# Optimization experiments

Measured on AMD Instinct MI355X. Metric: run time of the kernel, lower is better.

Reference implementation:

```python
import jax, jax.numpy as jnp
import numpy as np

B, S, HID = 1, 2048, 1024
H, HKV, D = 16, 4, 64
THETA = 10000.0


def _rope_tables(seq_len, head_dim):
    # Matches RotaryEmbedding: emb = cat(freqs, freqs); kernel reads cos/sin at even
    # positions d for each rotated pair (d, d+1), i.e. columns 0::2 of the table.
    inv_freq = 1.0 / (THETA ** (jnp.arange(0, head_dim, 2, dtype=jnp.float32) / head_dim))
    freqs = jnp.arange(seq_len, dtype=jnp.float32)[:, None] * inv_freq[None, :]  # [S, D/2]
    emb = jnp.concatenate([freqs, freqs], axis=-1)  # [S, D]
    return jnp.cos(emb)[:, 0::2], jnp.sin(emb)[:, 0::2]  # each [S, D/2]


def _apply_rope(x, cos, sin):
    # x: [B, H, S, D]; rotate interleaved pairs (2i, 2i+1) as in the kernel.
    xe, xo = x[..., 0::2], x[..., 1::2]
    re = xe * cos - xo * sin
    ro = xe * sin + xo * cos
    return jnp.stack([re, ro], axis=-1).reshape(x.shape)


def setup_inputs() -> dict:
    key = jax.random.key(0)
    k0, k1, k2, k3, k4 = jax.random.split(key, 5)
    return {
        "hidden_states": jax.random.normal(k0, (B, S, HID), dtype=jnp.float32),
        "Wq": jax.random.normal(k1, (HID, H * D), dtype=jnp.float32) * 0.02,
        "Wk": jax.random.normal(k2, (HID, HKV * D), dtype=jnp.float32) * 0.02,
        "Wv": jax.random.normal(k3, (HID, HKV * D), dtype=jnp.float32) * 0.02,
        "Wo": jax.random.normal(k4, (H * D, HID), dtype=jnp.float32) * 0.02,
    }


def reference(hidden_states, Wq, Wk, Wv, Wo):
    b, s, _ = hidden_states.shape
    q = (hidden_states @ Wq).reshape(b, s, H, D).transpose(0, 2, 1, 3)    # [B,H,S,D]
    k = (hidden_states @ Wk).reshape(b, s, HKV, D).transpose(0, 2, 1, 3)  # [B,Hkv,S,D]
    v = (hidden_states @ Wv).reshape(b, s, HKV, D).transpose(0, 2, 1, 3)

    cos, sin = _rope_tables(s, D)
    q = _apply_rope(q, cos, sin)
    k = _apply_rope(k, cos, sin)

    G = H // HKV  # GQA group size: query head h -> kv head h // G
    qg = q.reshape(b, HKV, G, s, D)
    scale = jnp.float32(D) ** -0.5
    scores = jnp.einsum("bkgqd,bkpd->bkgqp", qg, k) * scale  # [B,Hkv,G,S,S]
    causal = jnp.tril(jnp.ones((s, s), dtype=bool))
    scores = jnp.where(causal, scores, jnp.float32(-1e30))
    probs = jax.nn.softmax(scores, axis=-1)
    out = jnp.einsum("bkgqp,bkpd->bkgqd", probs, v).reshape(b, H, s, D)
    out = out.transpose(0, 2, 1, 3).reshape(b, s, H * D)
    return out @ Wo
```

## Files before the change

### kernel.cpp

```cpp
#include <hip/hip_runtime.h>
#include <hip/hip_bf16.h>
#include <math.h>

#define SEQ   2048
#define HID   1024
#define NH    16
#define NKV   4
#define DH    64
#define GQ    (NH / NKV)
#define NQKV  1536
#define KT    64
#define QB    32
#define CH    512
#define NCH   (SEQ / CH)
#define PSTR  72
#define LNSC  0.2878231366f

typedef __attribute__((ext_vector_type(8))) short bf16x8;
typedef __attribute__((ext_vector_type(4))) float f32x4;
typedef unsigned short u16;
typedef unsigned int u32;

__device__ __forceinline__ u16 f2bf(float f) {
    union { float f; unsigned u; } x; x.f = f;
    unsigned r = x.u + 0x7fffu + ((x.u >> 16) & 1u);
    return (u16)(r >> 16);
}
__device__ __forceinline__ u32 pk2bf(float lo, float hi) {
    return (u32)f2bf(lo) | ((u32)f2bf(hi) << 16);
}
__device__ __forceinline__ void load_lds16(const u16* g, u16* l) {
    __builtin_amdgcn_global_load_lds(
        (const __attribute__((address_space(1))) unsigned int*)g,
        (__attribute__((address_space(3))) unsigned int*)l, 16, 0, 0);
}

__global__ __launch_bounds__(256) void setup(const float* __restrict__ X,
                                             const float* __restrict__ Wq,
                                             const float* __restrict__ Wk,
                                             const float* __restrict__ Wv,
                                             const float* __restrict__ Wo,
                                             u16* __restrict__ Xb,
                                             u16* __restrict__ Wt,
                                             u16* __restrict__ WoT) {
    const int z = blockIdx.z;
    if (z == 4) {
        const int idx = ((int)blockIdx.y * 64 + (int)blockIdx.x) * 256 + threadIdx.x;
        const float4 v = ((const float4*)X)[idx];
        ushort4 o;
        o.x = f2bf(v.x); o.y = f2bf(v.y); o.z = f2bf(v.z); o.w = f2bf(v.w);
        ((ushort4*)Xb)[idx] = o;
        return;
    }
    const float* in; u16* out; int N;
    if (z == 0)      { in = Wq; out = Wt;                             N = HID; }
    else if (z == 1) { in = Wk; out = Wt + (size_t)HID * HID;         N = 256; }
    else if (z == 2) { in = Wv; out = Wt + (size_t)(HID + 256) * HID; N = 256; }
    else             { in = Wo; out = WoT;                            N = HID; }

    const int n0 = blockIdx.x * 32;
    if (n0 >= N) return;
    const int k0 = blockIdx.y * 32;

    __shared__ float t[32][33];
    const int tx = threadIdx.x & 31;
    const int ty = threadIdx.x >> 5;
    #pragma unroll
    for (int i = 0; i < 4; ++i)
        t[ty + i * 8][tx] = in[(size_t)(k0 + ty + i * 8) * N + n0 + tx];
    __syncthreads();
    #pragma unroll
    for (int i = 0; i < 4; ++i)
        out[(size_t)(n0 + ty + i * 8) * HID + k0 + tx] = f2bf(t[tx][ty + i * 8]);
}

__global__ __launch_bounds__(256) void gemm_qkv(const u16* __restrict__ A,
                                                const u16* __restrict__ Bt,
                                                u16* __restrict__ Qb,
                                                u16* __restrict__ Kb,
                                                u16* __restrict__ VTg) {
    __shared__ u16 Bs[2][64 * 32];

    const int tid  = threadIdx.x;
    const int lane = tid & 63;
    const int w    = tid >> 6;
    const int c    = lane & 15;
    const int quad = lane >> 4;
    const int m0   = blockIdx.y * 64;
    const int n0   = blockIdx.x * 64;

    const u16* gB  = Bt + (size_t)(n0 + w * 16 + (lane >> 2)) * HID + (lane & 3) * 8;
    u16* const bdst = (u16*)&Bs[0][0] + (w * 16) * 32;
    const u16* gA = A + (size_t)(m0 + w * 16 + c) * HID + quad * 8;

    f32x4 acc[4];
    #pragma unroll
    for (int nt = 0; nt < 4; ++nt) acc[nt] = (f32x4){0.f, 0.f, 0.f, 0.f};

    bf16x8 afc, afn;
    afc = *(const bf16x8*)gA;
    load_lds16(gB, bdst);

    for (int t = 0; t < HID / 32; ++t) {
        __syncthreads();
        if (t + 1 < HID / 32) {
            load_lds16(gB + (t + 1) * 32, bdst + ((t + 1) & 1) * (64 * 32));
            afn = *(const bf16x8*)(gA + (t + 1) * 32);
        }
        bf16x8 bfr[4];
        #pragma unroll
        for (int nt = 0; nt < 4; ++nt)
            bfr[nt] = *(const bf16x8*)&Bs[t & 1][(nt * 16 + c) * 32 + quad * 8];
        #pragma unroll
        for (int nt = 0; nt < 4; ++nt)
            acc[nt] = __builtin_amdgcn_mfma_f32_16x16x32_bf16(afc, bfr[nt], acc[nt], 0, 0, 0);
        afc = afn;
    }

    const int s0 = m0 + w * 16 + quad * 4;
    if (n0 < 1280) {
        const bool isQ = (n0 < 1024);
        #pragma unroll
        for (int nt = 0; nt < 4; ++nt) {
            const int d = nt * 16 + c;
            const float inv_freq = __expf(-(float)(d & 30) * LNSC);
            const float sgn = (d & 1) ? 1.f : -1.f;
            #pragma unroll
            for (int rg = 0; rg < 4; ++rg) {
                const float self = acc[nt][rg];
                const float partner = __shfl_xor(self, 1);
                float sn, cs;
                __sincosf((float)(s0 + rg) * inv_freq, &sn, &cs);
                float o = fmaf(partner, sgn * sn, self * cs);
                if (isQ) {
                    Qb[(size_t)(s0 + rg) * HID + n0 + d] = f2bf(o * 0.125f);
                } else {
                    const int kh = (n0 - 1024) >> 6;
                    Kb[((size_t)kh * SEQ + s0 + rg) * DH + d] = f2bf(o);
                }
            }
        }
    } else {
        const int kh = (n0 - 1280) >> 6;
        #pragma unroll
        for (int nt = 0; nt < 4; ++nt) {
            const int d = nt * 16 + c;
            ushort4 o;
            o.x = f2bf(acc[nt][0]); o.y = f2bf(acc[nt][1]);
            o.z = f2bf(acc[nt][2]); o.w = f2bf(acc[nt][3]);
            *(ushort4*)&VTg[((size_t)kh * DH + d) * SEQ + s0] = o;
        }
    }
}

__global__ __launch_bounds__(256) void gemm64(const u16* __restrict__ A,
                                              const u16* __restrict__ Bt,
                                              float* __restrict__ C,
                                              int K, int ldc) {
    __shared__ u16 Bs[2][64 * 32];

    const int tid  = threadIdx.x;
    const int lane = tid & 63;
    const int w    = tid >> 6;
    const int c    = lane & 15;
    const int quad = lane >> 4;
    const int m0   = blockIdx.y * 64;
    const int n0   = blockIdx.x * 64;

    const u16* gB  = Bt + (size_t)(n0 + w * 16 + (lane >> 2)) * K + (lane & 3) * 8;
    u16* const bdst = (u16*)&Bs[0][0] + (w * 16) * 32;
    const u16* gA = A + (size_t)(m0 + w * 16 + c) * K + quad * 8;

    const int T = K / 32;

    f32x4 acc[4];
    #pragma unroll
    for (int nt = 0; nt < 4; ++nt) acc[nt] = (f32x4){0.f, 0.f, 0.f, 0.f};

    bf16x8 afc, afn;
    afc = *(const bf16x8*)gA;
    load_lds16(gB, bdst);

    for (int t = 0; t < T; ++t) {
        __syncthreads();
        if (t + 1 < T) {
            load_lds16(gB + (t + 1) * 32, bdst + ((t + 1) & 1) * (64 * 32));
            afn = *(const bf16x8*)(gA + (t + 1) * 32);
        }
        bf16x8 bfr[4];
        #pragma unroll
        for (int nt = 0; nt < 4; ++nt)
            bfr[nt] = *(const bf16x8*)&Bs[t & 1][(nt * 16 + c) * 32 + quad * 8];
        #pragma unroll
        for (int nt = 0; nt < 4; ++nt)
            acc[nt] = __builtin_amdgcn_mfma_f32_16x16x32_bf16(afc, bfr[nt], acc[nt], 0, 0, 0);
        afc = afn;
    }

    #pragma unroll
    for (int nt = 0; nt < 4; ++nt)
        #pragma unroll
        for (int rg = 0; rg < 4; ++rg)
            C[(size_t)(m0 + w * 16 + quad * 4 + rg) * ldc + n0 + nt * 16 + c] = acc[nt][rg];
}

__global__ __launch_bounds__(256) void attn_kernel(const u16* __restrict__ Qb,
                                                   const u16* __restrict__ Kb,
                                                   const u16* __restrict__ VTg,
                                                   float* __restrict__ Opart,
                                                   float* __restrict__ lpart) {
    __shared__ u16 Ks[2][2][64 * 32];
    __shared__ u16 Vs[2][2][64 * 32];
    __shared__ u16 Pst[4][QB * PSTR];

    const int tid  = threadIdx.x;
    const int lane = tid & 63;
    const int w    = tid >> 6;
    const int c    = lane & 15;
    const int quad = lane >> 4;
    const int kh   = blockIdx.y;
    const int z    = blockIdx.z;
    const int qt   = (SEQ / QB - 1) - (int)blockIdx.x;
    const int q0   = qt * QB;
    const int h    = kh * GQ + w;

    const int kstart = z * CH;
    const int klim   = q0 + QB;
    if (kstart >= klim) return;
    const int kend   = (klim < kstart + CH) ? klim : (kstart + CH);
    const int ntiles = (kend - kstart + KT - 1) / KT;

    bf16x8 qf[2][2];
    #pragma unroll
    for (int g = 0; g < 2; ++g)
        #pragma unroll
        for (int ks = 0; ks < 2; ++ks)
            qf[g][ks] = *(const bf16x8*)&Qb[(size_t)(q0 + g * 16 + c) * HID + h * DH + ks * 32 + quad * 8];

    f32x4 accO[4][2];
    #pragma unroll
    for (int nt = 0; nt < 4; ++nt)
        #pragma unroll
        for (int g = 0; g < 2; ++g)
            accO[nt][g] = (f32x4){0.f, 0.f, 0.f, 0.f};
    float l[2] = {0.f, 0.f};

    const int hf = w >> 1;
    const int g0 = (w & 1) * 2;
    const int srow = (lane >> 2);
    const int scol = (lane & 3) * 8;

    {
        #pragma unroll
        for (int gi = 0; gi < 2; ++gi) {
            const int g = g0 + gi;
            load_lds16(Kb + ((size_t)kh * SEQ + kstart + g * 16 + srow) * DH + hf * 32 + scol,
                       &Ks[0][hf][(g * 16) * 32]);
            load_lds16(VTg + ((size_t)kh * DH + g * 16 + srow) * SEQ + kstart + hf * 32 + scol,
                       &Vs[0][hf][(g * 16) * 32]);
        }
    }

    for (int t = 0; t < ntiles; ++t) {
        const int kt0 = kstart + t * KT;
        __syncthreads();
        if (t + 1 < ntiles) {
            const int nk = kt0 + KT;
            const int nb = (t + 1) & 1;
            #pragma unroll
            for (int gi = 0; gi < 2; ++gi) {
                const int g = g0 + gi;
                load_lds16(Kb + ((size_t)kh * SEQ + nk + g * 16 + srow) * DH + hf * 32 + scol,
                           &Ks[nb][hf][(g * 16) * 32]);
                load_lds16(VTg + ((size_t)kh * DH + g * 16 + srow) * SEQ + nk + hf * 32 + scol,
                           &Vs[nb][hf][(g * 16) * 32]);
            }
        }
        const int b = t & 1;

        f32x4 accS[4][2];
        #pragma unroll
        for (int nS = 0; nS < 4; ++nS)
            #pragma unroll
            for (int g = 0; g < 2; ++g)
                accS[nS][g] = (f32x4){0.f, 0.f, 0.f, 0.f};
        #pragma unroll
        for (int nS = 0; nS < 4; ++nS)
            #pragma unroll
            for (int ks = 0; ks < 2; ++ks) {
                const bf16x8 kf = *(const bf16x8*)&Ks[b][ks][(nS * 16 + c) * 32 + quad * 8];
                #pragma unroll
                for (int g = 0; g < 2; ++g)
                    accS[nS][g] = __builtin_amdgcn_mfma_f32_16x16x32_bf16(kf, qf[g][ks], accS[nS][g], 0, 0, 0);
            }

        #pragma unroll
        for (int g = 0; g < 2; ++g) {
            const int q = q0 + g * 16 + c;
            #pragma unroll
            for (int nS = 0; nS < 4; ++nS) {
                const int key = kt0 + nS * 16 + quad * 4;
                const float p0 = (key + 0 <= q) ? __expf(accS[nS][g][0]) : 0.f;
                const float p1 = (key + 1 <= q) ? __expf(accS[nS][g][1]) : 0.f;
                const float p2 = (key + 2 <= q) ? __expf(accS[nS][g][2]) : 0.f;
                const float p3 = (key + 3 <= q) ? __expf(accS[nS][g][3]) : 0.f;
                l[g] += (p0 + p1) + (p2 + p3);
                u32* dst = (u32*)&Pst[w][(g * 16 + c) * PSTR + nS * 16 + quad * 4];
                dst[0] = pk2bf(p0, p1);
                dst[1] = pk2bf(p2, p3);
            }
        }
        __threadfence_block();

        #pragma unroll
        for (int ks2 = 0; ks2 < 2; ++ks2) {
            bf16x8 pf[2];
            #pragma unroll
            for (int g = 0; g < 2; ++g)
                pf[g] = *(const bf16x8*)&Pst[w][(g * 16 + c) * PSTR + ks2 * 32 + quad * 8];
            #pragma unroll
            for (int nt = 0; nt < 4; ++nt) {
                const bf16x8 vf = *(const bf16x8*)&Vs[b][ks2][(nt * 16 + c) * 32 + quad * 8];
                #pragma unroll
                for (int g = 0; g < 2; ++g)
                    accO[nt][g] = __builtin_amdgcn_mfma_f32_16x16x32_bf16(vf, pf[g], accO[nt][g], 0, 0, 0);
            }
        }
    }

    #pragma unroll
    for (int g = 0; g < 2; ++g) {
        float lg = l[g];
        lg += __shfl_xor(lg, 16);
        lg += __shfl_xor(lg, 32);
        if (quad == 0)
            lpart[((size_t)z * SEQ + q0 + g * 16 + c) * NH + h] = lg;

        float* Op = Opart + ((size_t)z * SEQ + q0 + g * 16 + c) * HID + h * DH;
        #pragma unroll
        for (int nt = 0; nt < 4; ++nt)
            *(f32x4*)&Op[nt * 16 + quad * 4] = accO[nt][g];
    }
}

__global__ __launch_bounds__(256) void attn_reduce(const float* __restrict__ Opart,
                                                   const float* __restrict__ lpart,
                                                   u16* __restrict__ At) {
    const int idx = blockIdx.x * 256 + threadIdx.x;
    const int q  = idx >> 8;
    const int h  = (idx & 255) >> 4;
    const int klim = (q & ~(QB - 1)) + QB;
    float4 o = ((const float4*)Opart)[idx];
    float  l = lpart[q * NH + h];
    #pragma unroll
    for (int z = 1; z < NCH; ++z) {
        if (z * CH < klim) {
            const float4 o1 = ((const float4*)Opart)[idx + z * (SEQ * HID / 4)];
            o.x += o1.x; o.y += o1.y; o.z += o1.z; o.w += o1.w;
            l += lpart[(z * SEQ + q) * NH + h];
        }
    }
    const float inv = 1.0f / l;
    ushort4 r;
    r.x = f2bf(o.x * inv); r.y = f2bf(o.y * inv);
    r.z = f2bf(o.z * inv); r.w = f2bf(o.w * inv);
    ((ushort4*)At)[idx] = r;
}

extern "C" void kernel_launch(void* const* d_in, const int* in_sizes, int n_in,
                              void* d_out, int out_size, void* d_ws, size_t ws_size,
                              hipStream_t stream) {
    const float* X  = (const float*)d_in[0];
    const float* Wq = (const float*)d_in[1];
    const float* Wk = (const float*)d_in[2];
    const float* Wv = (const float*)d_in[3];
    const float* Wo = (const float*)d_in[4];
    float* out = (float*)d_out;

    u16* Wt     = (u16*)d_ws;
    u16* WoT    = Wt + (size_t)NQKV * HID;
    u16* Xb     = WoT + (size_t)HID * HID;
    u16* At     = Xb + (size_t)SEQ * HID;
    u16* Qb     = At + (size_t)SEQ * HID;
    u16* Kb     = Qb + (size_t)SEQ * HID;
    u16* VTg    = Kb + (size_t)NKV * SEQ * DH;
    float* Opart = (float*)(VTg + (size_t)NKV * DH * SEQ);
    float* lpart = Opart + (size_t)NCH * SEQ * HID;

    dim3 blk(256);

    setup<<<dim3(64, 32, 5), blk, 0, stream>>>(X, Wq, Wk, Wv, Wo, Xb, Wt, WoT);

    gemm_qkv<<<dim3(NQKV / 64, SEQ / 64), blk, 0, stream>>>(Xb, Wt, Qb, Kb, VTg);

    attn_kernel<<<dim3(SEQ / QB, NKV, NCH), blk, 0, stream>>>(Qb, Kb, VTg, Opart, lpart);

    attn_reduce<<<(SEQ * HID / 4) / 256, blk, 0, stream>>>(Opart, lpart, At);

    gemm64<<<dim3(HID / 64, SEQ / 64), blk, 0, stream>>>(At, WoT, out, HID, HID);
}
```

Baseline: 141.1 us.

## Fuse split-K attention reduction into attention kernel via last-block atomic counter

Removes the separate attn_reduce launch. Query tiles covered by a single KV chunk now normalize and write bf16 output directly, with no fp32 partials. For multi-chunk tiles, each block writes its partials, then increments an atomic counter, and the last-arriving block sums the partials and writes the final output. This saves one kernel launch and the partial-buffer round trip for short-prefix tiles. The cost is threadfences, atomics, and a serialized reduction in the tail block. The counters are zeroed in the setup kernel.

New measurement: 239.6 us. 69.8% more time.

```diff
diff --git a/kernel.cpp b/kernel.cpp
--- a/kernel.cpp
+++ b/kernel.cpp
@@ -42,9 +42,12 @@
                                              const float* __restrict__ Wo,
                                              u16* __restrict__ Xb,
                                              u16* __restrict__ Wt,
-                                             u16* __restrict__ WoT) {
+                                             u16* __restrict__ WoT,
+                                             int* __restrict__ cnt) {
     const int z = blockIdx.z;
     if (z == 4) {
+        if (blockIdx.x == 0 && blockIdx.y == 0)
+            cnt[threadIdx.x] = 0;
         const int idx = ((int)blockIdx.y * 64 + (int)blockIdx.x) * 256 + threadIdx.x;
         const float4 v = ((const float4*)X)[idx];
         ushort4 o;
@@ -208,7 +211,9 @@
                                                    const u16* __restrict__ Kb,
                                                    const u16* __restrict__ VTg,
                                                    float* __restrict__ Opart,
-                                                   float* __restrict__ lpart) {
+                                                   float* __restrict__ lpart,
+                                                   int* __restrict__ cnt,
+                                                   u16* __restrict__ At) {
     __shared__ u16 Ks[2][2][64 * 32];
     __shared__ u16 Vs[2][2][64 * 32];
     __shared__ u16 Pst[4][QB * PSTR];
@@ -328,6 +333,29 @@
         }
     }
 
+    const int nchunks = (q0 + QB + CH - 1) / CH;
+
+    if (nchunks == 1) {
+        #pragma unroll
+        for (int g = 0; g < 2; ++g) {
+            float lg = l[g];
+            lg += __shfl_xor(lg, 16);
+            lg += __shfl_xor(lg, 32);
+            const float inv = 1.0f / lg;
+            u16* Ap = At + (size_t)(q0 + g * 16 + c) * HID + h * DH;
+            #pragma unroll
+            for (int nt = 0; nt < 4; ++nt) {
+                ushort4 o;
+                o.x = f2bf(accO[nt][g][0] * inv);
+                o.y = f2bf(accO[nt][g][1] * inv);
+                o.z = f2bf(accO[nt][g][2] * inv);
+                o.w = f2bf(accO[nt][g][3] * inv);
+                *(ushort4*)&Ap[nt * 16 + quad * 4] = o;
+            }
+        }
+        return;
+    }
+
     #pragma unroll
     for (int g = 0; g < 2; ++g) {
         float lg = l[g];
@@ -341,30 +369,31 @@
         for (int nt = 0; nt < 4; ++nt)
             *(f32x4*)&Op[nt * 16 + quad * 4] = accO[nt][g];
     }
-}
-
-__global__ __launch_bounds__(256) void attn_reduce(const float* __restrict__ Opart,
-                                                   const float* __restrict__ lpart,
-                                                   u16* __restrict__ At) {
-    const int idx = blockIdx.x * 256 + threadIdx.x;
-    const int q  = idx >> 8;
-    const int h  = (idx & 255) >> 4;
-    const int klim = (q & ~(QB - 1)) + QB;
-    float4 o = ((const float4*)Opart)[idx];
-    float  l = lpart[q * NH + h];
-    #pragma unroll
-    for (int z = 1; z < NCH; ++z) {
-        if (z * CH < klim) {
-            const float4 o1 = ((const float4*)Opart)[idx + z * (SEQ * HID / 4)];
-            o.x += o1.x; o.y += o1.y; o.z += o1.z; o.w += o1.w;
-            l += lpart[(z * SEQ + q) * NH + h];
-        }
-    }
-    const float inv = 1.0f / l;
-    ushort4 r;
-    r.x = f2bf(o.x * inv); r.y = f2bf(o.y * inv);
-    r.z = f2bf(o.z * inv); r.w = f2bf(o.w * inv);
-    ((ushort4*)At)[idx] = r;
+
+    __threadfence();
+    __shared__ int done;
+    if (tid == 0) done = atomicAdd(&cnt[qt * NKV + kh], 1);
+    __syncthreads();
+    if (done != nchunks - 1) return;
+    __threadfence();
+
+    const int col4 = tid & 63;
+    const int hcol = kh * (GQ * DH) + col4 * 4;
+    const int hh   = kh * GQ + (col4 >> 4);
+    for (int r = q0 + (tid >> 6); r < q0 + QB; r += 4) {
+        float4 o = {0.f, 0.f, 0.f, 0.f};
+        float lsum = 0.f;
+        for (int zz = 0; zz < nchunks; ++zz) {
+            const float4 p = *(const float4*)&Opart[((size_t)zz * SEQ + r) * HID + hcol];
+            o.x += p.x; o.y += p.y; o.z += p.z; o.w += p.w;
+            lsum += lpart[((size_t)zz * SEQ + r) * NH + hh];
+        }
+        const float inv = 1.0f / lsum;
+        ushort4 rr;
+        rr.x = f2bf(o.x * inv); rr.y = f2bf(o.y * inv);
+        rr.z = f2bf(o.z * inv); rr.w = f2bf(o.w * inv);
+        *(ushort4*)&At[(size_t)r * HID + hcol] = rr;
+    }
 }
 
 extern "C" void kernel_launch(void* const* d_in, const int* in_sizes, int n_in,
@@ -386,16 +415,15 @@
     u16* VTg    = Kb + (size_t)NKV * SEQ * DH;
     float* Opart = (float*)(VTg + (size_t)NKV * DH * SEQ);
     float* lpart = Opart + (size_t)NCH * SEQ * HID;
+    int*   cnt   = (int*)(lpart + (size_t)NCH * SEQ * NH);
 
     dim3 blk(256);
 
-    setup<<<dim3(64, 32, 5), blk, 0, stream>>>(X, Wq, Wk, Wv, Wo, Xb, Wt, WoT);
+    setup<<<dim3(64, 32, 5), blk, 0, stream>>>(X, Wq, Wk, Wv, Wo, Xb, Wt, WoT, cnt);
 
     gemm_qkv<<<dim3(NQKV / 64, SEQ / 64), blk, 0, stream>>>(Xb, Wt, Qb, Kb, VTg);
 
-    attn_kernel<<<dim3(SEQ / QB, NKV, NCH), blk, 0, stream>>>(Qb, Kb, VTg, Opart, lpart);
-
-    attn_reduce<<<(SEQ * HID / 4) / 256, blk, 0, stream>>>(Opart, lpart, At);
+    attn_kernel<<<dim3(SEQ / QB, NKV, NCH), blk, 0, stream>>>(Qb, Kb, VTg, Opart, lpart, cnt, At);
 
     gemm64<<<dim3(HID / 64, SEQ / 64), blk, 0, stream>>>(At, WoT, out, HID, HID);
 }
```

## Deepen GEMM K-tile to 64 with padded LDS, write single-chunk attention rows directly

Applied to the files above, without the earlier changes.

Both GEMM kernels now stage a K=64 slice of B per iteration into a padded LDS layout (row groups strided by 528 elements), so there are half as many barriers and each barrier covers twice as many MFMAs. The attention kernel gets an extra output pointer. Query tiles whose causal range fits in one 512-key chunk now normalise and write bf16 output straight to At, skipping the partial-buffer round trip. The reduce kernel is launched only over rows at or beyond position 512. This trades more LDS per block and more live registers for less synchronisation and less memory traffic.

New measurement: 135.8 us. 3.8% less time.

```diff
diff --git a/kernel.cpp b/kernel.cpp
--- a/kernel.cpp
+++ b/kernel.cpp
@@ -15,6 +15,8 @@
 #define NCH   (SEQ / CH)
 #define PSTR  72
 #define LNSC  0.2878231366f
+#define GS    528
+#define BUFS  (8 * GS)
 
 typedef __attribute__((ext_vector_type(8))) short bf16x8;
 typedef __attribute__((ext_vector_type(4))) float f32x4;
@@ -79,7 +81,7 @@
                                                 u16* __restrict__ Qb,
                                                 u16* __restrict__ Kb,
                                                 u16* __restrict__ VTg) {
-    __shared__ u16 Bs[2][64 * 32];
+    __shared__ u16 Bs[2 * BUFS];
 
     const int tid  = threadIdx.x;
     const int lane = tid & 63;
@@ -89,32 +91,47 @@
     const int m0   = blockIdx.y * 64;
     const int n0   = blockIdx.x * 64;
 
-    const u16* gB  = Bt + (size_t)(n0 + w * 16 + (lane >> 2)) * HID + (lane & 3) * 8;
-    u16* const bdst = (u16*)&Bs[0][0] + (w * 16) * 32;
+    const u16* gB0 = Bt + (size_t)(n0 + w * 16 + (lane >> 3)) * HID + (lane & 7) * 8;
+    const u16* gB1 = gB0 + (size_t)8 * HID;
+    const int  gofs0 = (w * 2) * GS, gofs1 = (w * 2 + 1) * GS;
+
     const u16* gA = A + (size_t)(m0 + w * 16 + c) * HID + quad * 8;
+    const int  bfoff = (c >> 3) * GS + (c & 7) * 64 + quad * 8;
 
     f32x4 acc[4];
     #pragma unroll
     for (int nt = 0; nt < 4; ++nt) acc[nt] = (f32x4){0.f, 0.f, 0.f, 0.f};
 
-    bf16x8 afc, afn;
-    afc = *(const bf16x8*)gA;
-    load_lds16(gB, bdst);
-
-    for (int t = 0; t < HID / 32; ++t) {
+    bf16x8 afc[2], afn[2];
+    afc[0] = *(const bf16x8*)gA;
+    afc[1] = *(const bf16x8*)(gA + 32);
+    load_lds16(gB0, &Bs[gofs0]);
+    load_lds16(gB1, &Bs[gofs1]);
+
+    const int T = HID / 64;
+    for (int t = 0; t < T; ++t) {
         __syncthreads();
-        if (t + 1 < HID / 32) {
-            load_lds16(gB + (t + 1) * 32, bdst + ((t + 1) & 1) * (64 * 32));
-            afn = *(const bf16x8*)(gA + (t + 1) * 32);
-        }
-        bf16x8 bfr[4];
+        if (t + 1 < T) {
+            const int nb = ((t + 1) & 1) * BUFS;
+            load_lds16(gB0 + (t + 1) * 64, &Bs[nb + gofs0]);
+            load_lds16(gB1 + (t + 1) * 64, &Bs[nb + gofs1]);
+            afn[0] = *(const bf16x8*)(gA + (t + 1) * 64);
+            afn[1] = *(const bf16x8*)(gA + (t + 1) * 64 + 32);
+        }
+        const int b = (t & 1) * BUFS;
+        bf16x8 bfr[4][2];
         #pragma unroll
         for (int nt = 0; nt < 4; ++nt)
-            bfr[nt] = *(const bf16x8*)&Bs[t & 1][(nt * 16 + c) * 32 + quad * 8];
-        #pragma unroll
-        for (int nt = 0; nt < 4; ++nt)
-            acc[nt] = __builtin_amdgcn_mfma_f32_16x16x32_bf16(afc, bfr[nt], acc[nt], 0, 0, 0);
-        afc = afn;
+            #pragma unroll
+            for (int ks = 0; ks < 2; ++ks)
+                bfr[nt][ks] = *(const bf16x8*)&Bs[b + nt * (2 * GS) + ks * 32 + bfoff];
+        #pragma unroll
+        for (int ks = 0; ks < 2; ++ks)
+            #pragma unroll
+            for (int nt = 0; nt < 4; ++nt)
+                acc[nt] = __builtin_amdgcn_mfma_f32_16x16x32_bf16(afc[ks], bfr[nt][ks], acc[nt], 0, 0, 0);
+        afc[0] = afn[0];
+        afc[1] = afn[1];
     }
 
     const int s0 = m0 + w * 16 + quad * 4;
@@ -157,7 +174,7 @@
                                               const u16* __restrict__ Bt,
                                               float* __restrict__ C,
                                               int K, int ldc) {
-    __shared__ u16 Bs[2][64 * 32];
+    __shared__ u16 Bs[2 * BUFS];
 
     const int tid  = threadIdx.x;
     const int lane = tid & 63;
@@ -167,34 +184,47 @@
     const int m0   = blockIdx.y * 64;
     const int n0   = blockIdx.x * 64;
 
-    const u16* gB  = Bt + (size_t)(n0 + w * 16 + (lane >> 2)) * K + (lane & 3) * 8;
-    u16* const bdst = (u16*)&Bs[0][0] + (w * 16) * 32;
+    const u16* gB0 = Bt + (size_t)(n0 + w * 16 + (lane >> 3)) * K + (lane & 7) * 8;
+    const u16* gB1 = gB0 + (size_t)8 * K;
+    const int  gofs0 = (w * 2) * GS, gofs1 = (w * 2 + 1) * GS;
+
     const u16* gA = A + (size_t)(m0 + w * 16 + c) * K + quad * 8;
-
-    const int T = K / 32;
+    const int  bfoff = (c >> 3) * GS + (c & 7) * 64 + quad * 8;
 
     f32x4 acc[4];
     #pragma unroll
     for (int nt = 0; nt < 4; ++nt) acc[nt] = (f32x4){0.f, 0.f, 0.f, 0.f};
 
-    bf16x8 afc, afn;
-    afc = *(const bf16x8*)gA;
-    load_lds16(gB, bdst);
-
+    bf16x8 afc[2], afn[2];
+    afc[0] = *(const bf16x8*)gA;
+    afc[1] = *(const bf16x8*)(gA + 32);
+    load_lds16(gB0, &Bs[gofs0]);
+    load_lds16(gB1, &Bs[gofs1]);
+
+    const int T = K / 64;
     for (int t = 0; t < T; ++t) {
         __syncthreads();
         if (t + 1 < T) {
-            load_lds16(gB + (t + 1) * 32, bdst + ((t + 1) & 1) * (64 * 32));
-            afn = *(const bf16x8*)(gA + (t + 1) * 32);
-        }
-        bf16x8 bfr[4];
+            const int nb = ((t + 1) & 1) * BUFS;
+            load_lds16(gB0 + (t + 1) * 64, &Bs[nb + gofs0]);
+            load_lds16(gB1 + (t + 1) * 64, &Bs[nb + gofs1]);
+            afn[0] = *(const bf16x8*)(gA + (t + 1) * 64);
+            afn[1] = *(const bf16x8*)(gA + (t + 1) * 64 + 32);
+        }
+        const int b = (t & 1) * BUFS;
+        bf16x8 bfr[4][2];
         #pragma unroll
         for (int nt = 0; nt < 4; ++nt)
-            bfr[nt] = *(const bf16x8*)&Bs[t & 1][(nt * 16 + c) * 32 + quad * 8];
-        #pragma unroll
-        for (int nt = 0; nt < 4; ++nt)
-            acc[nt] = __builtin_amdgcn_mfma_f32_16x16x32_bf16(afc, bfr[nt], acc[nt], 0, 0, 0);
-        afc = afn;
+            #pragma unroll
+            for (int ks = 0; ks < 2; ++ks)
+                bfr[nt][ks] = *(const bf16x8*)&Bs[b + nt * (2 * GS) + ks * 32 + bfoff];
+        #pragma unroll
+        for (int ks = 0; ks < 2; ++ks)
+            #pragma unroll
+            for (int nt = 0; nt < 4; ++nt)
+                acc[nt] = __builtin_amdgcn_mfma_f32_16x16x32_bf16(afc[ks], bfr[nt][ks], acc[nt], 0, 0, 0);
+        afc[0] = afn[0];
+        afc[1] = afn[1];
     }
 
     #pragma unroll
@@ -208,7 +238,8 @@
                                                    const u16* __restrict__ Kb,
                                                    const u16* __restrict__ VTg,
                                                    float* __restrict__ Opart,
-                                                   float* __restrict__ lpart) {
+                                                   float* __restrict__ lpart,
+                                                   u16* __restrict__ At) {
     __shared__ u16 Ks[2][2][64 * 32];
     __shared__ u16 Vs[2][2][64 * 32];
     __shared__ u16 Pst[4][QB * PSTR];
@@ -328,6 +359,29 @@
         }
     }
 
+    const int nchunks = (q0 + QB + CH - 1) / CH;
+
+    if (nchunks == 1) {
+        #pragma unroll
+        for (int g = 0; g < 2; ++g) {
+            float lg = l[g];
+            lg += __shfl_xor(lg, 16);
+            lg += __shfl_xor(lg, 32);
+            const float inv = 1.0f / lg;
+            u16* Ap = At + (size_t)(q0 + g * 16 + c) * HID + h * DH;
+            #pragma unroll
+            for (int nt = 0; nt < 4; ++nt) {
+                ushort4 o;
+                o.x = f2bf(accO[nt][g][0] * inv);
+                o.y = f2bf(accO[nt][g][1] * inv);
+                o.z = f2bf(accO[nt][g][2] * inv);
+                o.w = f2bf(accO[nt][g][3] * inv);
+                *(ushort4*)&Ap[nt * 16 + quad * 4] = o;
+            }
+        }
+        return;
+    }
+
     #pragma unroll
     for (int g = 0; g < 2; ++g) {
         float lg = l[g];
@@ -346,7 +400,7 @@
 __global__ __launch_bounds__(256) void attn_reduce(const float* __restrict__ Opart,
                                                    const float* __restrict__ lpart,
                                                    u16* __restrict__ At) {
-    const int idx = blockIdx.x * 256 + threadIdx.x;
+    const int idx = blockIdx.x * 256 + threadIdx.x + (CH * HID / 4);
     const int q  = idx >> 8;
     const int h  = (idx & 255) >> 4;
     const int klim = (q & ~(QB - 1)) + QB;
@@ -393,9 +447,9 @@
 
     gemm_qkv<<<dim3(NQKV / 64, SEQ / 64), blk, 0, stream>>>(Xb, Wt, Qb, Kb, VTg);
 
-    attn_kernel<<<dim3(SEQ / QB, NKV, NCH), blk, 0, stream>>>(Qb, Kb, VTg, Opart, lpart);
-
-    attn_reduce<<<(SEQ * HID / 4) / 256, blk, 0, stream>>>(Opart, lpart, At);
+    attn_kernel<<<dim3(SEQ / QB, NKV, NCH), blk, 0, stream>>>(Qb, Kb, VTg, Opart, lpart, At);
+
+    attn_reduce<<<((SEQ - CH) * HID / 4) / 256, blk, 0, stream>>>(Opart, lpart, At);
 
     gemm64<<<dim3(HID / 64, SEQ / 64), blk, 0, stream>>>(At, WoT, out, HID, HID);
 }
```
